# Kernel tuning notes

Hardware: AMD Instinct MI355X
Metric: run time of the kernel (lower is better)

## Reference

```python
import jax, jax.numpy as jnp
import numpy as np

B, T, N = 256, 2048, 64
START_IDX, END_IDX = 1, 2  # mead Offsets.GO, Offsets.EOS
NEG_INF = -10000.0


def setup_inputs() -> dict:
    key = jax.random.key(0)
    k1, k2, k3 = jax.random.split(key, 3)
    unary = jax.random.normal(k1, (B, T, N), dtype=jnp.float32)
    trans = jax.random.normal(k2, (N, N), dtype=jnp.float32) * 0.1  # [to_tag, from_tag]
    lengths = jax.random.randint(k3, (B,), T // 2, T + 1, dtype=jnp.int32)
    return {"unary": unary, "trans": trans, "lengths": lengths}


def reference(unary, trans, lengths):
    """CRF forward algorithm (partition function), batch_first input.

    unary: [B, T, N] emission scores
    trans: [N, N]    trans[j, k] = score of transitioning from tag k to tag j
    lengths: [B]     valid sequence lengths
    returns: [B]     log partition scores
    """
    unary_tbn = jnp.transpose(unary, (1, 0, 2))  # [T, B, N]
    n_tags = trans.shape[0]

    alphas0 = jnp.full((unary.shape[0], n_tags), NEG_INF, dtype=unary.dtype)
    alphas0 = alphas0.at[:, START_IDX].set(0.0)

    def step(alphas, inp):
        unary_t, t = inp  # unary_t: [B, N]
        # scores[b, j, k] = alphas[b, k] + trans[j, k] + unary_t[b, j]
        scores = alphas[:, None, :] + trans[None, :, :] + unary_t[:, :, None]
        new_alphas = jax.nn.logsumexp(scores, axis=2)  # [B, N]
        alphas = jnp.where((t < lengths)[:, None], new_alphas, alphas)
        return alphas, None

    alphas, _ = jax.lax.scan(step, alphas0, (unary_tbn, jnp.arange(T, dtype=lengths.dtype)))
    terminal = alphas + trans[END_IDX][None, :]  # transitions into EOS
    return jax.nn.logsumexp(terminal, axis=1)  # [B]
```

## Files before the change

### kernel.cpp

```cpp
#include <hip/hip_runtime.h>


typedef __attribute__((ext_vector_type(4))) float f32x4;
typedef __attribute__((ext_vector_type(8))) short bf16x8;

namespace {
constexpr int kB = 256;
constexpr int kT = 2048;
constexpr int kN = 64;
constexpr int kC = 8;
constexpr int kL = kT / kC;
constexpr int kStart = 1;
constexpr int kEnd = 2;
constexpr long kTileFloats = (long)kB * kC * 4 * 1024;
constexpr long kNumTiles = (long)kB * kC * 4;
}

__device__ __forceinline__ unsigned pack2bf(float lo, float hi) {
  return __builtin_amdgcn_perm(__float_as_uint(hi), __float_as_uint(lo), 0x07060302u);
}

__device__ __forceinline__ f32x4 expand2(unsigned u, unsigned v) {
  f32x4 e;
  e.x = __uint_as_float(u << 16);
  e.y = __uint_as_float(u & 0xFFFF0000u);
  e.z = __uint_as_float(v << 16);
  e.w = __uint_as_float(v & 0xFFFF0000u);
  return e;
}

__device__ __forceinline__ f32x4 exp4(f32x4 v) {
  f32x4 r;
  r.x = __expf(v.x);
  r.y = __expf(v.y);
  r.z = __expf(v.z);
  r.w = __expf(v.w);
  return r;
}

__device__ __forceinline__ float exp2i(int d) {
  return (d <= -127) ? 0.f : __uint_as_float((unsigned)(127 + d) << 23);
}

__device__ __forceinline__ float scr_rd(const char* scr, int scrStride, long F) {
  return *(const float*)(scr + (F >> 5) * (long)scrStride + (F & 31) * 4);
}

__device__ __forceinline__ void step32(f32x4 (&ps)[2][4], const bf16x8 (&af)[4][2],
                                       const char* lrow) {
  const f32x4 e0 = *(const f32x4*)(lrow + 0);
  const f32x4 e1 = *(const f32x4*)(lrow + 16);
  const f32x4 e2 = *(const f32x4*)(lrow + 32);
  const f32x4 e3 = *(const f32x4*)(lrow + 48);
  const f32x4 z4 = {0.f, 0.f, 0.f, 0.f};
#pragma unroll
  for (int nt = 0; nt < 2; ++nt) {
    union { unsigned u[4]; bf16x8 s; } b0u, b1u;
    b0u.u[0] = pack2bf(ps[nt][0].x, ps[nt][0].y);
    b0u.u[1] = pack2bf(ps[nt][0].z, ps[nt][0].w);
    b0u.u[2] = pack2bf(ps[nt][1].x, ps[nt][1].y);
    b0u.u[3] = pack2bf(ps[nt][1].z, ps[nt][1].w);
    b1u.u[0] = pack2bf(ps[nt][2].x, ps[nt][2].y);
    b1u.u[1] = pack2bf(ps[nt][2].z, ps[nt][2].w);
    b1u.u[2] = pack2bf(ps[nt][3].x, ps[nt][3].y);
    b1u.u[3] = pack2bf(ps[nt][3].z, ps[nt][3].w);
    const bf16x8 b0 = b0u.s, b1 = b1u.s;
    f32x4 q0 = __builtin_amdgcn_mfma_f32_16x16x32_bf16(af[0][0], b0, z4, 0, 0, 0);
    f32x4 q1 = __builtin_amdgcn_mfma_f32_16x16x32_bf16(af[1][0], b0, z4, 0, 0, 0);
    f32x4 q2 = __builtin_amdgcn_mfma_f32_16x16x32_bf16(af[2][0], b0, z4, 0, 0, 0);
    f32x4 q3 = __builtin_amdgcn_mfma_f32_16x16x32_bf16(af[3][0], b0, z4, 0, 0, 0);
    q0 = __builtin_amdgcn_mfma_f32_16x16x32_bf16(af[0][1], b1, q0, 0, 0, 0);
    q1 = __builtin_amdgcn_mfma_f32_16x16x32_bf16(af[1][1], b1, q1, 0, 0, 0);
    q2 = __builtin_amdgcn_mfma_f32_16x16x32_bf16(af[2][1], b1, q2, 0, 0, 0);
    q3 = __builtin_amdgcn_mfma_f32_16x16x32_bf16(af[3][1], b1, q3, 0, 0, 0);
    ps[nt][0] = q0 * e0;
    ps[nt][1] = q1 * e1;
    ps[nt][2] = q2 * e2;
    ps[nt][3] = q3 * e3;
  }
}

__device__ __forceinline__ void renorm32(f32x4 (&ps)[2][4], float& tot_e) {
  const unsigned eref = __builtin_amdgcn_readfirstlane(__float_as_uint(ps[0][0].x));
  const int e = (int)((eref >> 23) & 0xFFu) - 127;
  const float sc = __uint_as_float((unsigned)(127 - e) << 23);
#pragma unroll
  for (int nt = 0; nt < 2; ++nt)
#pragma unroll
    for (int mt = 0; mt < 4; ++mt) ps[nt][mt] *= sc;
  tot_e += (float)e;
}

__global__ __launch_bounds__(64, 3) void chunk32_kernel(
    const char* __restrict__ un, const float* __restrict__ trans,
    const int* __restrict__ lengths, char* __restrict__ scr, int scrStride) {
  const int bid = blockIdx.x;
  const int b = bid >> 4;
  const int c = (bid >> 1) & 7;
  const int h = bid & 1;
  const int len = lengths[b];
  const int start = c * kL;
  int steps = len - start;
  if (steps <= 0) return;
  if (steps > kL) steps = kL;

  const int lane = threadIdx.x & 63;
  const int col = lane & 15;
  const int q4 = lane >> 4;

  bf16x8 af[4][2];
#pragma unroll
  for (int mt = 0; mt < 4; ++mt) {
#pragma unroll
    for (int kc = 0; kc < 2; ++kc) {
      union { unsigned u[4]; bf16x8 s; } fr;
#pragma unroll
      for (int jp = 0; jp < 4; ++jp) {
        const int j0 = 2 * jp, j1 = 2 * jp + 1;
        const int k0 = (2 * kc + (j0 >> 2)) * 16 + q4 * 4 + (j0 & 3);
        const int k1 = (2 * kc + (j1 >> 2)) * 16 + q4 * 4 + (j1 & 3);
        unsigned e0 = __float_as_uint(__expf(trans[(mt * 16 + col) * kN + k0])) + 0x8000u;
        unsigned e1 = __float_as_uint(__expf(trans[(mt * 16 + col) * kN + k1])) + 0x8000u;
        fr.u[jp] = __builtin_amdgcn_perm(e1, e0, 0x07060302u);
      }
      af[mt][kc] = fr.s;
    }
  }

  f32x4 ps[2][4];
#pragma unroll
  for (int nt = 0; nt < 2; ++nt) {
    const int mycol = h * 32 + nt * 16 + col;
#pragma unroll
    for (int mt = 0; mt < 4; ++mt) {
      const int rb = mt * 16 + q4 * 4;
      f32x4 v;
      v.x = (rb + 0 == mycol) ? 1.f : 0.f;
      v.y = (rb + 1 == mycol) ? 1.f : 0.f;
      v.z = (rb + 2 == mycol) ? 1.f : 0.f;
      v.w = (rb + 3 == mycol) ? 1.f : 0.f;
      ps[nt][mt] = v;
    }
  }

  const char* gbase = un + (size_t)(b * kT + start) * 256;
  const int srow = lane >> 2;
  const int sb = lane & 3;
  const size_t gRow = (size_t)srow * 256;

  __shared__ __align__(16) char sm[2][4096];

  {
    const char* g = gbase + gRow + sb * 16;
    f32x4 v0 = exp4(*(const f32x4*)(g + 0));
    f32x4 v1 = exp4(*(const f32x4*)(g + 64));
    f32x4 v2 = exp4(*(const f32x4*)(g + 128));
    f32x4 v3 = exp4(*(const f32x4*)(g + 192));
    char* l = &sm[0][0] + gRow + (size_t)sb * 64;
    *(f32x4*)(l + 0) = v0;
    *(f32x4*)(l + 16) = v1;
    *(f32x4*)(l + 32) = v2;
    *(f32x4*)(l + 48) = v3;
  }

  float tot_e = 0.0f;
  const int nst = (steps + 15) >> 4;
  for (int s = 0; s < nst; ++s) {
    f32x4 v0, v1, v2, v3;
    const bool more = (s + 1 < nst);
    if (more) {
      const char* g = gbase + (size_t)(s + 1) * 4096 + gRow + sb * 16;
      v0 = *(const f32x4*)(g + 0);
      v1 = *(const f32x4*)(g + 64);
      v2 = *(const f32x4*)(g + 128);
      v3 = *(const f32x4*)(g + 192);
    }

    int ns = steps - s * 16;
    ns = ns > 16 ? 16 : ns;
    const char* lb = &sm[s & 1][0] + q4 * 64;
    if (ns == 16) {
      const char* l2 = lb;
#pragma unroll 1
      for (int g4 = 0; g4 < 4; ++g4) {
        step32(ps, af, l2 + 0);
        step32(ps, af, l2 + 256);
        step32(ps, af, l2 + 512);
        step32(ps, af, l2 + 768);
        renorm32(ps, tot_e);
        l2 += 1024;
      }
    } else {
      for (int i = 0; i < ns; ++i) {
        step32(ps, af, lb + (size_t)i * 256);
        if ((i & 3) == 3) renorm32(ps, tot_e);
      }
    }

    if (more) {
      char* l = &sm[(s + 1) & 1][0] + gRow + (size_t)sb * 64;
      *(f32x4*)(l + 0) = exp4(v0);
      *(f32x4*)(l + 16) = exp4(v1);
      *(f32x4*)(l + 32) = exp4(v2);
      *(f32x4*)(l + 48) = exp4(v3);
    }
  }

  const long tbase = ((long)b * kC + c) * 4 + h * 2;
#pragma unroll
  for (int nt = 0; nt < 2; ++nt) {
    const long tileIdx = tbase + nt;
#pragma unroll
    for (int mt = 0; mt < 4; ++mt) {
      const long slot = tileIdx * 32 + col * 2 + (mt >> 1);
      char* addr = scr + slot * (long)scrStride + ((mt & 1) * 16 + q4 * 4) * 4;
      *(f32x4*)addr = ps[nt][mt];
    }
    if (lane == 0) {
      const long F = kTileFloats + tileIdx;
      *(float*)(scr + (F >> 5) * (long)scrStride + (F & 31) * 4) = tot_e;
    }
  }
}

__device__ __forceinline__ void load_mat(const char* scr, int scrStride, long tb,
                                         int j, float (&m)[4][16], float (&ev)[4]) {
#pragma unroll
  for (int s = 0; s < 4; ++s) {
#pragma unroll
    for (int k = 0; k < 16; ++k)
      m[s][k] = scr_rd(scr, scrStride, (tb + s) * 1024 + (long)k * 64 + j);
    ev[s] = scr_rd(scr, scrStride, kTileFloats + tb + s);
  }
}

__global__ __launch_bounds__(64, 1) void combine_kernel(
    const char* __restrict__ scr, int scrStride, const float* __restrict__ trans,
    const int* __restrict__ lengths, float* __restrict__ out) {
  const int b = blockIdx.x;
  const int j = threadIdx.x;
  const int len = lengths[b];

  const long t0 = (long)b * kC * 4;
  float a = scr_rd(scr, scrStride, t0 * 1024 + kStart * 64 + j);
  float totE = scr_rd(scr, scrStride, kTileFloats + t0);

  float mc[4][16], ec[4];
  load_mat(scr, scrStride, t0 + 4, j, mc, ec);

#pragma unroll
  for (int c = 1; c < kC; ++c) {
    float mn[4][16], en[4];
    if (c + 1 < kC)
      load_mat(scr, scrStride, t0 + (long)(c + 1) * 4, j, mn, en);

    if (c * kL < len) {
      float s0 = 0.f, s1 = 0.f, s2 = 0.f, s3 = 0.f;
#pragma unroll
      for (int k16 = 0; k16 < 16; ++k16) {
        const float a0 = __int_as_float(__builtin_amdgcn_readlane(__float_as_int(a), k16));
        const float a1 = __int_as_float(__builtin_amdgcn_readlane(__float_as_int(a), 16 + k16));
        const float a2 = __int_as_float(__builtin_amdgcn_readlane(__float_as_int(a), 32 + k16));
        const float a3 = __int_as_float(__builtin_amdgcn_readlane(__float_as_int(a), 48 + k16));
        s0 = fmaf(mc[0][k16], a0, s0);
        s1 = fmaf(mc[1][k16], a1, s1);
        s2 = fmaf(mc[2][k16], a2, s2);
        s3 = fmaf(mc[3][k16], a3, s3);
      }
      const float em = fmaxf(fmaxf(ec[0], ec[1]), fmaxf(ec[2], ec[3]));
      a = s0 * exp2i((int)(ec[0] - em)) + s1 * exp2i((int)(ec[1] - em)) +
          s2 * exp2i((int)(ec[2] - em)) + s3 * exp2i((int)(ec[3] - em));
      totE += em;

      float m = a;
#pragma unroll
      for (int mask = 1; mask < 64; mask <<= 1) m = fmaxf(m, __shfl_xor(m, mask));
      const int e = (int)((__float_as_uint(m) >> 23) & 0xFFu) - 127;
      a *= exp2i(-e);
      totE += (float)e;
    }

    if (c + 1 < kC) {
#pragma unroll
      for (int s = 0; s < 4; ++s) {
#pragma unroll
        for (int k = 0; k < 16; ++k) mc[s][k] = mn[s][k];
        ec[s] = en[s];
      }
    }
  }

  float term = a * __expf(trans[kEnd * kN + j]);
#pragma unroll
  for (int mask = 1; mask < 64; mask <<= 1) term += __shfl_xor(term, mask);

  if (j == 0) out[b] = totE * 0.69314718055994530942f + logf(term);
}

__global__ void exp_swizzle_bf16(const float* in, char* outbase) {
  const int total = kB * kT * 32;
  int p = blockIdx.x * blockDim.x + threadIdx.x;
  const int stride = gridDim.x * blockDim.x;
  for (; p < total; p += stride) {
    const int r = p >> 5;
    const int j0 = (p & 31) << 1;
    const float2 v = *(const float2*)(in + (size_t)r * kN + j0);
    const float e0 = __expf(v.x), e1 = __expf(v.y);
    unsigned u0 = __float_as_uint(e0);
    u0 += 0x7FFFu + ((u0 >> 16) & 1u);
    unsigned u1 = __float_as_uint(e1);
    u1 += 0x7FFFu + ((u1 >> 16) & 1u);
    const unsigned d = (u1 & 0xFFFF0000u) | (u0 >> 16);
    const int pi = ((j0 >> 2) & 3) * 16 + ((j0 >> 4) << 2) + (j0 & 3);
    *(unsigned*)(outbase + (size_t)r * 256 + pi * 2) = d;
  }
}

__device__ __forceinline__ void step_lds_bf16(f32x4 (&ps)[4], const bf16x8 (&af)[4][2],
                                              const char* lrow) {
  const uint4 u0 = *(const uint4*)(lrow + 0);
  const uint4 u1 = *(const uint4*)(lrow + 16);
  f32x4 e0 = expand2(u0.x, u0.y);
  f32x4 e1 = expand2(u0.z, u0.w);
  f32x4 e2 = expand2(u1.x, u1.y);
  f32x4 e3 = expand2(u1.z, u1.w);

  union { unsigned u[4]; bf16x8 s; } b0u, b1u;
  b0u.u[0] = pack2bf(ps[0].x, ps[0].y);
  b0u.u[1] = pack2bf(ps[0].z, ps[0].w);
  b0u.u[2] = pack2bf(ps[1].x, ps[1].y);
  b0u.u[3] = pack2bf(ps[1].z, ps[1].w);
  const bf16x8 b0 = b0u.s;
  const f32x4 z4 = {0.f, 0.f, 0.f, 0.f};
  f32x4 q0 = __builtin_amdgcn_mfma_f32_16x16x32_bf16(af[0][0], b0, z4, 0, 0, 0);
  f32x4 q1 = __builtin_amdgcn_mfma_f32_16x16x32_bf16(af[1][0], b0, z4, 0, 0, 0);
  f32x4 q2 = __builtin_amdgcn_mfma_f32_16x16x32_bf16(af[2][0], b0, z4, 0, 0, 0);
  f32x4 q3 = __builtin_amdgcn_mfma_f32_16x16x32_bf16(af[3][0], b0, z4, 0, 0, 0);
  b1u.u[0] = pack2bf(ps[2].x, ps[2].y);
  b1u.u[1] = pack2bf(ps[2].z, ps[2].w);
  b1u.u[2] = pack2bf(ps[3].x, ps[3].y);
  b1u.u[3] = pack2bf(ps[3].z, ps[3].w);
  const bf16x8 b1 = b1u.s;
  q0 = __builtin_amdgcn_mfma_f32_16x16x32_bf16(af[0][1], b1, q0, 0, 0, 0);
  q1 = __builtin_amdgcn_mfma_f32_16x16x32_bf16(af[1][1], b1, q1, 0, 0, 0);
  q2 = __builtin_amdgcn_mfma_f32_16x16x32_bf16(af[2][1], b1, q2, 0, 0, 0);
  q3 = __builtin_amdgcn_mfma_f32_16x16x32_bf16(af[3][1], b1, q3, 0, 0, 0);

  ps[0] = q0 * e0;
  ps[1] = q1 * e1;
  ps[2] = q2 * e2;
  ps[3] = q3 * e3;
}

__device__ __forceinline__ void renorm16(f32x4 (&ps)[4], float& tot_e) {
  const unsigned eref = __builtin_amdgcn_readfirstlane(__float_as_uint(ps[0].x));
  const int e = (int)((eref >> 23) & 0xFFu) - 127;
  const float sc = __uint_as_float((unsigned)(127 - e) << 23);
#pragma unroll
  for (int mt = 0; mt < 4; ++mt) ps[mt] *= sc;
  tot_e += (float)e;
}

__global__ __launch_bounds__(256, 3) void chunk_pair_bf16_kernel(
    const char* __restrict__ eu, const float* __restrict__ trans,
    const int* __restrict__ lengths, char* __restrict__ scr, int scrStride) {
  constexpr int RB = 128;
  constexpr int SEG = RB / 8;
  constexpr int STG = 32 * RB;

  const int b = blockIdx.x >> 2;
  const int cp = blockIdx.x & 3;
  const int len = lengths[b];
  const int cA = 2 * cp, cB = 2 * cp + 1;
  int stepsA = len - cA * kL;
  stepsA = stepsA < 0 ? 0 : (stepsA > kL ? kL : stepsA);
  int stepsB = len - cB * kL;
  stepsB = stepsB < 0 ? 0 : (stepsB > kL ? kL : stepsB);
  if (stepsA <= 0) return;

  const int t8 = threadIdx.x;
  const int lane = t8 & 63;
  const int w = t8 >> 6;
  const int col = lane & 15;
  const int q4 = lane >> 4;

  bf16x8 af[4][2];
#pragma unroll
  for (int mt = 0; mt < 4; ++mt) {
#pragma unroll
    for (int kc = 0; kc < 2; ++kc) {
      union { unsigned u[4]; bf16x8 s; } fr;
#pragma unroll
      for (int jp = 0; jp < 4; ++jp) {
        const int j0 = 2 * jp, j1 = 2 * jp + 1;
        const int k0 = (2 * kc + (j0 >> 2)) * 16 + q4 * 4 + (j0 & 3);
        const int k1 = (2 * kc + (j1 >> 2)) * 16 + q4 * 4 + (j1 & 3);
        unsigned e0 = __float_as_uint(__expf(trans[(mt * 16 + col) * kN + k0])) + 0x8000u;
        unsigned e1 = __float_as_uint(__expf(trans[(mt * 16 + col) * kN + k1])) + 0x8000u;
        fr.u[jp] = __builtin_amdgcn_perm(e1, e0, 0x07060302u);
      }
      af[mt][kc] = fr.s;
    }
  }

  const int mycol = w * 16 + col;
  f32x4 psA[4], psB[4];
#pragma unroll
  for (int mt = 0; mt < 4; ++mt) {
    const int rb = mt * 16 + q4 * 4;
    f32x4 v;
    v.x = (rb + 0 == mycol) ? 1.f : 0.f;
    v.y = (rb + 1 == mycol) ? 1.f : 0.f;
    v.z = (rb + 2 == mycol) ? 1.f : 0.f;
    v.w = (rb + 3 == mycol) ? 1.f : 0.f;
    psA[mt] = v;
    psB[mt] = v;
  }

  const char* gblkA = eu + (size_t)(b * kT + cA * kL) * 256;
  const char* gblkB = eu + (size_t)(b * kT + cB * kL) * 256;
  const size_t gOff = (size_t)(t8 >> 3) * 256 + (size_t)(t8 & 7) * SEG;
  const size_t lOff = (size_t)(t8 >> 3) * RB + (size_t)(t8 & 7) * SEG;

  __shared__ __align__(16) char smem[2][2][STG];

  {
    uint4 vaA = *(const uint4*)(gblkA + gOff);
    uint4 vaB = *(const uint4*)(gblkB + gOff);
    *(uint4*)(&smem[0][0][0] + lOff) = vaA;
    *(uint4*)(&smem[1][0][0] + lOff) = vaB;
  }
  __syncthreads();

  float totA = 0.0f, totB = 0.0f;
  for (int s = 0; s < 8; ++s) {
    uint4 vaA, vaB;
    const bool more = (s < 7);
    if (more) {
      vaA = *(const uint4*)(gblkA + (size_t)(s + 1) * 8192 + gOff);
      vaB = *(const uint4*)(gblkB + (size_t)(s + 1) * 8192 + gOff);
    }

    int nsA = stepsA - s * 32;
    nsA = nsA < 0 ? 0 : (nsA > 32 ? 32 : nsA);
    int nsB = stepsB - s * 32;
    nsB = nsB < 0 ? 0 : (nsB > 32 ? 32 : nsB);
    const char* lbA = &smem[0][s & 1][0] + q4 * (RB / 4);
    const char* lbB = &smem[1][s & 1][0] + q4 * (RB / 4);

    if (nsA == 32 && nsB == 32) {
      for (int g = 0; g < 8; ++g) {
#pragma unroll
        for (int k = 0; k < 4; ++k) {
          step_lds_bf16(psA, af, lbA + (g * 4 + k) * RB);
          step_lds_bf16(psB, af, lbB + (g * 4 + k) * RB);
        }
        renorm16(psA, totA);
        renorm16(psB, totB);
      }
    } else {
      for (int i = 0; i < nsA; ++i) {
        step_lds_bf16(psA, af, lbA + (size_t)i * RB);
        if ((i & 3) == 3) renorm16(psA, totA);
      }
      for (int i = 0; i < nsB; ++i) {
        step_lds_bf16(psB, af, lbB + (size_t)i * RB);
        if ((i & 3) == 3) renorm16(psB, totB);
      }
    }

    if (more) {
      *(uint4*)(&smem[0][(s + 1) & 1][0] + lOff) = vaA;
      *(uint4*)(&smem[1][(s + 1) & 1][0] + lOff) = vaB;
    }
    __syncthreads();
  }

  {
    const long tileIdx = ((long)b * kC + cA) * 4 + w;
#pragma unroll
    for (int mt = 0; mt < 4; ++mt) {
      const long slot = tileIdx * 32 + col * 2 + (mt >> 1);
      char* addr = scr + slot * (long)scrStride + ((mt & 1) * 16 + q4 * 4) * 4;
      *(f32x4*)addr = psA[mt];
    }
    if (lane == 0) {
      const long F = kTileFloats + tileIdx;
      *(float*)(scr + (F >> 5) * (long)scrStride + (F & 31) * 4) = totA;
    }
  }
  if (stepsB > 0) {
    const long tileIdx = ((long)b * kC + cB) * 4 + w;
#pragma unroll
    for (int mt = 0; mt < 4; ++mt) {
      const long slot = tileIdx * 32 + col * 2 + (mt >> 1);
      char* addr = scr + slot * (long)scrStride + ((mt & 1) * 16 + q4 * 4) * 4;
      *(f32x4*)addr = psB[mt];
    }
    if (lane == 0) {
      const long F = kTileFloats + tileIdx;
      *(float*)(scr + (F >> 5) * (long)scrStride + (F & 31) * 4) = totB;
    }
  }
}

extern "C" void kernel_launch(void* const* d_in, const int* in_sizes, int n_in,
                              void* d_out, int out_size, void* d_ws, size_t ws_size,
                              hipStream_t stream) {
  const float* unary = (const float*)d_in[0];
  const float* trans = (const float*)d_in[1];
  const int* lengths = (const int*)d_in[2];
  float* out = (float*)d_out;

  const size_t scrBytes = (size_t)(kTileFloats + kNumTiles) * 4;

  if (ws_size >= scrBytes) {
    chunk32_kernel<<<dim3(kB * kC * 2), dim3(64), 0, stream>>>(
        (const char*)d_in[0], trans, lengths, (char*)d_ws, 128);
    combine_kernel<<<dim3(kB), dim3(64), 0, stream>>>((const char*)d_ws, 128,
                                                      trans, lengths, out);
  } else {
    exp_swizzle_bf16<<<dim3(4096), dim3(256), 0, stream>>>(unary, (char*)d_in[0]);
    chunk_pair_bf16_kernel<<<dim3(kB * 4), dim3(256), 0, stream>>>(
        (const char*)d_in[0], trans, lengths, (char*)d_in[0] + 128, 256);
    combine_kernel<<<dim3(kB), dim3(64), 0, stream>>>((const char*)d_in[0] + 128,
                                                      256, trans, lengths, out);
  }
}
```

Baseline: 391.8 us.

## Fuse chunk and combine kernels via per-batch atomic completion counters

Merges the separate combine kernel into the chunk kernel. Each block bumps a per-batch atomic counter after writing its tile, and the last-finishing block for a batch runs the combine step. This removes a kernel launch and the grid-wide dependency, so combine work can overlap with other batches' chunk work. In exchange it adds a memset launch, threadfences and atomics, and the combine now reads scratch inline without register prefetch.

```diff
diff --git a/kernel.cpp b/kernel.cpp
--- a/kernel.cpp
+++ b/kernel.cpp
@@ -91,9 +91,56 @@
   tot_e += (float)e;
 }
 
-__global__ __launch_bounds__(64, 3) void chunk32_kernel(
+__device__ __forceinline__ void combine_batch(const char* scr, int scrStride,
+                                              const float* trans, int len, int b,
+                                              float* out, int j) {
+  const long t0 = (long)b * kC * 4;
+  float a = scr_rd(scr, scrStride, t0 * 1024 + kStart * 64 + j);
+  float totE = scr_rd(scr, scrStride, kTileFloats + t0);
+
+  for (int c = 1; c < kC; ++c) {
+    if (c * kL >= len) break;
+    const long tb = t0 + (long)c * 4;
+    float s0 = 0.f, s1 = 0.f, s2 = 0.f, s3 = 0.f;
+#pragma unroll
+    for (int k16 = 0; k16 < 16; ++k16) {
+      const float a0 = __shfl(a, k16);
+      const float a1 = __shfl(a, 16 + k16);
+      const float a2 = __shfl(a, 32 + k16);
+      const float a3 = __shfl(a, 48 + k16);
+      s0 = fmaf(scr_rd(scr, scrStride, (tb + 0) * 1024 + k16 * 64 + j), a0, s0);
+      s1 = fmaf(scr_rd(scr, scrStride, (tb + 1) * 1024 + k16 * 64 + j), a1, s1);
+      s2 = fmaf(scr_rd(scr, scrStride, (tb + 2) * 1024 + k16 * 64 + j), a2, s2);
+      s3 = fmaf(scr_rd(scr, scrStride, (tb + 3) * 1024 + k16 * 64 + j), a3, s3);
+    }
+    const float e0 = scr_rd(scr, scrStride, kTileFloats + tb + 0);
+    const float e1 = scr_rd(scr, scrStride, kTileFloats + tb + 1);
+    const float e2 = scr_rd(scr, scrStride, kTileFloats + tb + 2);
+    const float e3 = scr_rd(scr, scrStride, kTileFloats + tb + 3);
+    const float em = fmaxf(fmaxf(e0, e1), fmaxf(e2, e3));
+    a = s0 * exp2i((int)(e0 - em)) + s1 * exp2i((int)(e1 - em)) +
+        s2 * exp2i((int)(e2 - em)) + s3 * exp2i((int)(e3 - em));
+    totE += em;
+
+    float m = a;
+#pragma unroll
+    for (int mask = 1; mask < 64; mask <<= 1) m = fmaxf(m, __shfl_xor(m, mask));
+    const int e = (int)((__float_as_uint(m) >> 23) & 0xFFu) - 127;
+    a *= exp2i(-e);
+    totE += (float)e;
+  }
+
+  float term = a * __expf(trans[kEnd * kN + j]);
+#pragma unroll
+  for (int mask = 1; mask < 64; mask <<= 1) term += __shfl_xor(term, mask);
+
+  if (j == 0) out[b] = totE * 0.69314718055994530942f + logf(term);
+}
+
+__global__ __launch_bounds__(64, 3) void fused_kernel(
     const char* __restrict__ un, const float* __restrict__ trans,
-    const int* __restrict__ lengths, char* __restrict__ scr, int scrStride) {
+    const int* __restrict__ lengths, char* __restrict__ scr, int scrStride,
+    int* __restrict__ counters, float* __restrict__ out) {
   const int bid = blockIdx.x;
   const int b = bid >> 4;
   const int c = (bid >> 1) & 7;
@@ -221,80 +268,16 @@
       *(float*)(scr + (F >> 5) * (long)scrStride + (F & 31) * 4) = tot_e;
     }
   }
-}
-
-__device__ __forceinline__ void load_mat(const char* scr, int scrStride, long tb,
-                                         int j, float (&m)[4][16], float (&ev)[4]) {
-#pragma unroll
-  for (int s = 0; s < 4; ++s) {
-#pragma unroll
-    for (int k = 0; k < 16; ++k)
-      m[s][k] = scr_rd(scr, scrStride, (tb + s) * 1024 + (long)k * 64 + j);
-    ev[s] = scr_rd(scr, scrStride, kTileFloats + tb + s);
-  }
-}
-
-__global__ __launch_bounds__(64, 1) void combine_kernel(
-    const char* __restrict__ scr, int scrStride, const float* __restrict__ trans,
-    const int* __restrict__ lengths, float* __restrict__ out) {
-  const int b = blockIdx.x;
-  const int j = threadIdx.x;
-  const int len = lengths[b];
-
-  const long t0 = (long)b * kC * 4;
-  float a = scr_rd(scr, scrStride, t0 * 1024 + kStart * 64 + j);
-  float totE = scr_rd(scr, scrStride, kTileFloats + t0);
-
-  float mc[4][16], ec[4];
-  load_mat(scr, scrStride, t0 + 4, j, mc, ec);
-
-#pragma unroll
-  for (int c = 1; c < kC; ++c) {
-    float mn[4][16], en[4];
-    if (c + 1 < kC)
-      load_mat(scr, scrStride, t0 + (long)(c + 1) * 4, j, mn, en);
-
-    if (c * kL < len) {
-      float s0 = 0.f, s1 = 0.f, s2 = 0.f, s3 = 0.f;
-#pragma unroll
-      for (int k16 = 0; k16 < 16; ++k16) {
-        const float a0 = __int_as_float(__builtin_amdgcn_readlane(__float_as_int(a), k16));
-        const float a1 = __int_as_float(__builtin_amdgcn_readlane(__float_as_int(a), 16 + k16));
-        const float a2 = __int_as_float(__builtin_amdgcn_readlane(__float_as_int(a), 32 + k16));
-        const float a3 = __int_as_float(__builtin_amdgcn_readlane(__float_as_int(a), 48 + k16));
-        s0 = fmaf(mc[0][k16], a0, s0);
-        s1 = fmaf(mc[1][k16], a1, s1);
-        s2 = fmaf(mc[2][k16], a2, s2);
-        s3 = fmaf(mc[3][k16], a3, s3);
-      }
-      const float em = fmaxf(fmaxf(ec[0], ec[1]), fmaxf(ec[2], ec[3]));
-      a = s0 * exp2i((int)(ec[0] - em)) + s1 * exp2i((int)(ec[1] - em)) +
-          s2 * exp2i((int)(ec[2] - em)) + s3 * exp2i((int)(ec[3] - em));
-      totE += em;
-
-      float m = a;
-#pragma unroll
-      for (int mask = 1; mask < 64; mask <<= 1) m = fmaxf(m, __shfl_xor(m, mask));
-      const int e = (int)((__float_as_uint(m) >> 23) & 0xFFu) - 127;
-      a *= exp2i(-e);
-      totE += (float)e;
-    }
-
-    if (c + 1 < kC) {
-#pragma unroll
-      for (int s = 0; s < 4; ++s) {
-#pragma unroll
-        for (int k = 0; k < 16; ++k) mc[s][k] = mn[s][k];
-        ec[s] = en[s];
-      }
-    }
-  }
-
-  float term = a * __expf(trans[kEnd * kN + j]);
-#pragma unroll
-  for (int mask = 1; mask < 64; mask <<= 1) term += __shfl_xor(term, mask);
-
-  if (j == 0) out[b] = totE * 0.69314718055994530942f + logf(term);
+
+  __threadfence();
+  int old = 0;
+  if (lane == 0) old = atomicAdd(&counters[b], 1);
+  old = __shfl(old, 0);
+  const int nact = (len + kL - 1) / kL;
+  if (old + 1 == 2 * nact) {
+    __threadfence();
+    combine_batch(scr, scrStride, trans, len, b, out, lane);
+  }
 }
 
 __global__ void exp_swizzle_bf16(const float* in, char* outbase) {
@@ -504,6 +487,14 @@
   }
 }
 
+__global__ __launch_bounds__(64) void combine_kernel(
+    const char* __restrict__ scr, int scrStride, const float* __restrict__ trans,
+    const int* __restrict__ lengths, float* __restrict__ out) {
+  const int b = blockIdx.x;
+  const int j = threadIdx.x;
+  combine_batch(scr, scrStride, trans, lengths[b], b, out, j);
+}
+
 extern "C" void kernel_launch(void* const* d_in, const int* in_sizes, int n_in,
                               void* d_out, int out_size, void* d_ws, size_t ws_size,
                               hipStream_t stream) {
@@ -513,12 +504,13 @@
   float* out = (float*)d_out;
 
   const size_t scrBytes = (size_t)(kTileFloats + kNumTiles) * 4;
-
-  if (ws_size >= scrBytes) {
-    chunk32_kernel<<<dim3(kB * kC * 2), dim3(64), 0, stream>>>(
-        (const char*)d_in[0], trans, lengths, (char*)d_ws, 128);
-    combine_kernel<<<dim3(kB), dim3(64), 0, stream>>>((const char*)d_ws, 128,
-                                                      trans, lengths, out);
+  const size_t cntBytes = (size_t)kB * sizeof(int);
+
+  if (ws_size >= scrBytes + cntBytes) {
+    int* counters = (int*)((char*)d_ws + scrBytes);
+    hipMemsetAsync(counters, 0, cntBytes, stream);
+    fused_kernel<<<dim3(kB * kC * 2), dim3(64), 0, stream>>>(
+        (const char*)d_in[0], trans, lengths, (char*)d_ws, 128, counters, out);
   } else {
     exp_swizzle_bf16<<<dim3(4096), dim3(256), 0, stream>>>(unary, (char*)d_in[0]);
     chunk_pair_bf16_kernel<<<dim3(kB * 4), dim3(256), 0, stream>>>(
```

New measurement: 642.7 us. 64.0% more time.
